# Kernel tuning notes

Measured on AMD Instinct MI355X. Metric: run time of the kernel, lower is better.

## Reference

```python
import jax, jax.numpy as jnp
import numpy as np

N, E, F, H, G, C = 50000, 800000, 768, 256, 512, 2  # H = nhid*2 (nhid=128), G graphs, C classes
NHID = 128


def setup_inputs() -> dict:
    key = jax.random.key(0)
    ks = jax.random.split(key, 18)
    s = 0.05
    x = jax.random.normal(ks[0], (N, F), jnp.float32)
    edge_index = jax.random.randint(ks[1], (2, E), 0, N, dtype=jnp.int32)
    # sorted batch vector; every graph non-empty so the 'first node per graph' gather is valid
    batch = ((jnp.arange(N) * G) // N).astype(jnp.int32)
    return {
        "x": x,
        "edge_index": edge_index,
        "batch": batch,
        # GATConv 1 (in=F, out=H, heads=1)
        "W1": jax.random.normal(ks[2], (F, H), jnp.float32) * s,
        "as1": jax.random.normal(ks[3], (H,), jnp.float32) * s,
        "ad1": jax.random.normal(ks[4], (H,), jnp.float32) * s,
        "b1": jnp.zeros((H,), jnp.float32),
        # GATConv 2 (in=H, out=H)
        "W2": jax.random.normal(ks[5], (H, H), jnp.float32) * s,
        "as2": jax.random.normal(ks[6], (H,), jnp.float32) * s,
        "ad2": jax.random.normal(ks[7], (H,), jnp.float32) * s,
        "b2": jnp.zeros((H,), jnp.float32),
        # fc0: num_features -> nhid (news branch)
        "W0": jax.random.normal(ks[8], (F, NHID), jnp.float32) * s,
        "b0": jnp.zeros((NHID,), jnp.float32),
        # fc1: 2*nhid -> nhid (used twice, as in the source)
        "Wf1": jax.random.normal(ks[9], (H, NHID), jnp.float32) * s,
        "bf1": jnp.zeros((NHID,), jnp.float32),
        # fc2: nhid -> num_classes
        "Wf2": jax.random.normal(ks[10], (NHID, C), jnp.float32) * s,
        "bf2": jnp.zeros((C,), jnp.float32),
    }


def _gat(x, src, dst, W, a_s, a_d, b):
    # PyG GATConv, heads=1, concat=True, negative_slope=0.2, self-loops pre-appended to src/dst.
    h = x @ W                                   # [N, H]
    e = jax.nn.leaky_relu((h @ a_s)[src] + (h @ a_d)[dst], 0.2)  # [E+N]
    m = jax.ops.segment_max(e, dst, num_segments=N)
    ex = jnp.exp(e - m[dst])                    # stable segment softmax numerator
    denom = jax.ops.segment_sum(ex, dst, num_segments=N)
    agg = jax.ops.segment_sum(ex[:, None] * h[src], dst, num_segments=N)  # [N, H]
    return agg / denom[:, None] + b


def reference(x, edge_index, batch, W1, as1, ad1, b1, W2, as2, ad2, b2, W0, b0, Wf1, bf1, Wf2, bf2):
    loop = jnp.arange(N, dtype=edge_index.dtype)
    src = jnp.concatenate([edge_index[0], loop])  # add self-loops (PyG default)
    dst = jnp.concatenate([edge_index[1], loop])
    h = jax.nn.selu(_gat(x, src, dst, W1, as1, ad1, b1))
    h = jax.nn.selu(_gat(h, src, dst, W2, as2, ad2, b2))
    # global mean pool over graphs
    cnt = jax.ops.segment_sum(jnp.ones((N,), h.dtype), batch, num_segments=G)
    pooled = jax.nn.selu(jax.ops.segment_sum(h, batch, num_segments=G) / cnt[:, None])
    z = jax.nn.selu(pooled @ Wf1 + bf1)
    # dropout(p=0.5) in eval mode -> identity
    # concat branch: first node of each graph (news root)
    first_idx = jax.ops.segment_min(jnp.arange(N), batch, num_segments=G)
    news = jax.nn.relu(x[first_idx] @ W0 + b0)
    z = jnp.concatenate([z, news], axis=1)       # [G, 2*nhid]
    z = jax.nn.relu(z @ Wf1 + bf1)
    return jax.nn.log_softmax(z @ Wf2 + bf2, axis=-1)
```

## Files before the change

kernel.cpp:

```cpp
#include <hip/hip_runtime.h>
#include <hip/hip_bf16.h>
#include <cstdint>
#include <cstddef>

#define NN 50000
#define EE 800000
#define FF 768
#define HH 256
#define GG 512
#define CC 2
#define NHIDD 128
#define ETOT (EE + NN)
#define NCHUNK 49

typedef __attribute__((ext_vector_type(8))) short bf16x8;
typedef __attribute__((ext_vector_type(4))) float f32x4;
typedef __attribute__((ext_vector_type(8))) unsigned short us8;

__device__ __forceinline__ float b2f(unsigned short u){
  union { float f; uint32_t i; } v; v.i = ((uint32_t)u) << 16; return v.f;
}
__device__ __forceinline__ unsigned short f2b(float f){
  uint32_t u = __float_as_uint(f);
  uint32_t r = (u + 0x7fffu + ((u >> 16) & 1u)) >> 16;
  return (unsigned short)r;
}
__device__ __forceinline__ float selu_f(float x){
  const float lam = 1.0507009873554805f, alp = 1.6732632423543772f;
  return x > 0.f ? lam * x : lam * alp * (__expf(x) - 1.f);
}

__global__ __launch_bounds__(256) void swizzleW(const float* __restrict__ W,
                                                unsigned short* __restrict__ Wsw, int K){
  int i = blockIdx.x * 256 + threadIdx.x;
  if (i < K * HH){
    int k = i / HH, n = i % HH;
    Wsw[(size_t)(k >> 5) * 8192 + n * 32 + (k & 31)] = f2b(W[i]);
  }
}

__global__ __launch_bounds__(256) void zero_deg(int* deg){
  int i = blockIdx.x * 256 + threadIdx.x;
  if (i < NN) deg[i] = 0;
}

__global__ __launch_bounds__(256) void deg_kernel(const int* __restrict__ dstA, int* __restrict__ deg){
  int i = blockIdx.x * 256 + threadIdx.x;
  if (i < ETOT){
    int d = (i < EE) ? dstA[i] : (i - EE);
    atomicAdd(&deg[d], 1);
  }
}

__global__ __launch_bounds__(256) void scanA(const int* __restrict__ deg, int* __restrict__ bsum){
  __shared__ int red[256];
  int c = blockIdx.x, tid = threadIdx.x;
  int base = c * 1024 + tid * 4;
  int s = 0;
#pragma unroll
  for (int j = 0; j < 4; j++){ int idx = base + j; if (idx < NN) s += deg[idx]; }
  red[tid] = s; __syncthreads();
  for (int off = 128; off > 0; off >>= 1){
    if (tid < off) red[tid] += red[tid + off];
    __syncthreads();
  }
  if (tid == 0) bsum[c] = red[0];
}

__global__ void scanB(int* bsum){
  if (threadIdx.x == 0){
    int run = 0;
    for (int i = 0; i < NCHUNK; i++){ int v = bsum[i]; bsum[i] = run; run += v; }
  }
}

__global__ __launch_bounds__(256) void scanC(const int* __restrict__ deg, const int* __restrict__ bsum,
                                             int* __restrict__ row_ptr, int* __restrict__ fill_ptr){
  __shared__ int ts[256];
  int c = blockIdx.x, tid = threadIdx.x;
  int base = c * 1024 + tid * 4;
  int v[4]; int s = 0;
#pragma unroll
  for (int j = 0; j < 4; j++){ int idx = base + j; v[j] = (idx < NN) ? deg[idx] : 0; s += v[j]; }
  ts[tid] = s; __syncthreads();
  for (int off = 1; off < 256; off <<= 1){
    int add = (tid >= off) ? ts[tid - off] : 0;
    __syncthreads();
    ts[tid] += add;
    __syncthreads();
  }
  int run = ts[tid] - s + bsum[c];
#pragma unroll
  for (int j = 0; j < 4; j++){
    int idx = base + j;
    if (idx < NN){ row_ptr[idx] = run; fill_ptr[idx] = run; }
    run += v[j];
  }
  if (c == 0 && tid == 0) row_ptr[NN] = ETOT;
}

__global__ __launch_bounds__(256) void fill_kernel(const int* __restrict__ srcA, const int* __restrict__ dstA,
                                                   int* __restrict__ fill_ptr, int* __restrict__ csr_src){
  int i = blockIdx.x * 256 + threadIdx.x;
  if (i < ETOT){
    int s = (i < EE) ? srcA[i] : (i - EE);
    int d = (i < EE) ? dstA[i] : (i - EE);
    int pos = atomicAdd(&fill_ptr[d], 1);
    csr_src[pos] = s;
  }
}

template<int K, bool AF32>
__global__ __launch_bounds__(256) void gemm_mfma(const void* __restrict__ Ap,
                                                 const unsigned short* __restrict__ Wsw,
                                                 unsigned short* __restrict__ out, int M){
  __shared__ unsigned short Al[64][40];
  __shared__ unsigned short Bl[256][40];
  const int tid = threadIdx.x;
  const int m0 = blockIdx.x * 64;
  const int lane = tid & 63, w = tid >> 6;
  const int koff = (lane >> 4) * 8;
  const int arow = lane & 15, bcol0 = w * 64 + (lane & 15);
  f32x4 acc[4][4];
#pragma unroll
  for (int rt = 0; rt < 4; rt++)
#pragma unroll
    for (int ct = 0; ct < 4; ct++) acc[rt][ct] = (f32x4){0.f, 0.f, 0.f, 0.f};

  const int srow = tid >> 2, skc = (tid & 3) * 8;
  for (int ks = 0; ks < K / 32; ks++){
    if (m0 + srow < M){
      if (AF32){
        const float* Af = (const float*)Ap;
        size_t ab = (size_t)(m0 + srow) * K + ks * 32 + skc;
        float4 f0 = *(const float4*)&Af[ab];
        float4 f1 = *(const float4*)&Af[ab + 4];
        us8 v;
        v[0] = f2b(f0.x); v[1] = f2b(f0.y); v[2] = f2b(f0.z); v[3] = f2b(f0.w);
        v[4] = f2b(f1.x); v[5] = f2b(f1.y); v[6] = f2b(f1.z); v[7] = f2b(f1.w);
        *(us8*)&Al[srow][skc] = v;
      } else {
        const unsigned short* Au = (const unsigned short*)Ap;
        *(us8*)&Al[srow][skc] = *(const us8*)&Au[(size_t)(m0 + srow) * K + ks * 32 + skc];
      }
    } else {
      us8 z = {0,0,0,0,0,0,0,0}; *(us8*)&Al[srow][skc] = z;
    }
    const unsigned short* wp = Wsw + (size_t)ks * 8192 + tid * 32;
    *(us8*)&Bl[tid][0]  = *(const us8*)&wp[0];
    *(us8*)&Bl[tid][8]  = *(const us8*)&wp[8];
    *(us8*)&Bl[tid][16] = *(const us8*)&wp[16];
    *(us8*)&Bl[tid][24] = *(const us8*)&wp[24];
    __syncthreads();
    bf16x8 af[4], bfr[4];
#pragma unroll
    for (int rt = 0; rt < 4; rt++) af[rt] = *(const bf16x8*)&Al[rt * 16 + arow][koff];
#pragma unroll
    for (int ct = 0; ct < 4; ct++) bfr[ct] = *(const bf16x8*)&Bl[bcol0 + ct * 16][koff];
#pragma unroll
    for (int rt = 0; rt < 4; rt++)
#pragma unroll
      for (int ct = 0; ct < 4; ct++)
        acc[rt][ct] = __builtin_amdgcn_mfma_f32_16x16x32_bf16(af[rt], bfr[ct], acc[rt][ct], 0, 0, 0);
    __syncthreads();
  }
#pragma unroll
  for (int rt = 0; rt < 4; rt++){
    int mbase = m0 + rt * 16 + (lane >> 4) * 4;
#pragma unroll
    for (int r = 0; r < 4; r++){
      int m = mbase + r;
      if (m < M){
        size_t ro = (size_t)m * HH + w * 64 + (lane & 15);
        out[ro + 0]  = f2b(acc[rt][0][r]);
        out[ro + 16] = f2b(acc[rt][1][r]);
        out[ro + 32] = f2b(acc[rt][2][r]);
        out[ro + 48] = f2b(acc[rt][3][r]);
      }
    }
  }
}

__global__ __launch_bounds__(256) void alsald_kernel(const unsigned short* __restrict__ h,
    const float* __restrict__ a_s, const float* __restrict__ a_d,
    float* __restrict__ als, float* __restrict__ ald){
  int node = blockIdx.x * 4 + (threadIdx.x >> 6);
  int lane = threadIdx.x & 63;
  if (node >= NN) return;
  ushort4 hv = *(const ushort4*)&h[(size_t)node * HH + lane * 4];
  float4 as4 = *(const float4*)&a_s[lane * 4];
  float4 ad4 = *(const float4*)&a_d[lane * 4];
  float h0 = b2f(hv.x), h1 = b2f(hv.y), h2 = b2f(hv.z), h3 = b2f(hv.w);
  float s = h0 * as4.x + h1 * as4.y + h2 * as4.z + h3 * as4.w;
  float d = h0 * ad4.x + h1 * ad4.y + h2 * ad4.z + h3 * ad4.w;
  for (int off = 32; off > 0; off >>= 1){ s += __shfl_xor(s, off); d += __shfl_xor(d, off); }
  if (lane == 0){ als[node] = s; ald[node] = d; }
}

__global__ __launch_bounds__(256) void agg_wave(const unsigned short* __restrict__ h,
    const float* __restrict__ als, const float* __restrict__ ald,
    const int* __restrict__ row_ptr, const int* __restrict__ csr_src,
    const float* __restrict__ bias, unsigned short* __restrict__ outp){
  int node = blockIdx.x * 4 + (threadIdx.x >> 6);
  int lane = threadIdx.x & 63;
  if (node >= NN) return;
  int base = row_ptr[node];
  int deg  = row_ptr[node + 1] - base;
  float aldd = ald[node];
  float den = 0.f;
  float a0 = 0.f, a1 = 0.f, a2 = 0.f, a3 = 0.f;
  const size_t fo = (size_t)lane * 4;
  for (int p0 = 0; p0 < deg; p0 += 64){
    int cnt = min(64, deg - p0);
    float ev = 0.f; int s = 0;
    if (lane < cnt){
      s = csr_src[base + p0 + lane];
      float v = als[s] + aldd;
      v = v > 0.f ? v : 0.2f * v;
      ev = __expf(v);
    }
    den += ev;
    int j = 0;
    for (; j + 2 <= cnt; j += 2){
      float e0 = __shfl(ev, j), e1 = __shfl(ev, j + 1);
      int s0 = __shfl(s, j), s1 = __shfl(s, j + 1);
      ushort4 g0 = *(const ushort4*)&h[(size_t)s0 * HH + fo];
      ushort4 g1 = *(const ushort4*)&h[(size_t)s1 * HH + fo];
      a0 += e0 * b2f(g0.x) + e1 * b2f(g1.x);
      a1 += e0 * b2f(g0.y) + e1 * b2f(g1.y);
      a2 += e0 * b2f(g0.z) + e1 * b2f(g1.z);
      a3 += e0 * b2f(g0.w) + e1 * b2f(g1.w);
    }
    for (; j < cnt; j++){
      float e0 = __shfl(ev, j); int s0 = __shfl(s, j);
      ushort4 g0 = *(const ushort4*)&h[(size_t)s0 * HH + fo];
      a0 += e0 * b2f(g0.x); a1 += e0 * b2f(g0.y); a2 += e0 * b2f(g0.z); a3 += e0 * b2f(g0.w);
    }
  }
  for (int off = 32; off > 0; off >>= 1) den += __shfl_xor(den, off);
  float inv = 1.f / den;
  float4 b4 = *(const float4*)&bias[fo];
  ushort4 o;
  o.x = f2b(selu_f(a0 * inv + b4.x));
  o.y = f2b(selu_f(a1 * inv + b4.y));
  o.z = f2b(selu_f(a2 * inv + b4.z));
  o.w = f2b(selu_f(a3 * inv + b4.w));
  *(ushort4*)&outp[(size_t)node * HH + fo] = o;
}

__global__ __launch_bounds__(256) void first_kernel(const int* __restrict__ batch, int* __restrict__ first_idx){
  int n = blockIdx.x * 256 + threadIdx.x;
  if (n < NN){
    int b = batch[n];
    if (n == 0 || batch[n - 1] != b) first_idx[b] = n;
  }
  if (blockIdx.x == 0 && threadIdx.x == 0) first_idx[GG] = NN;
}

__global__ __launch_bounds__(256) void pool_kernel(const unsigned short* __restrict__ x3,
    const int* __restrict__ first_idx, float* __restrict__ pooled){
  int g = blockIdx.x, f = threadIdx.x;
  int s = first_idx[g], e = first_idx[g + 1];
  float acc = 0.f;
  for (int n = s; n < e; n++) acc += b2f(x3[(size_t)n * HH + f]);
  pooled[g * HH + f] = selu_f(acc / (float)(e - s));
}

__global__ __launch_bounds__(128) void z1_kernel(const float* __restrict__ pooled,
    const float* __restrict__ Wf1, const float* __restrict__ bf1,
    float* __restrict__ z1){
  __shared__ float pr[HH];
  int g = blockIdx.x, t = threadIdx.x;
  pr[t] = pooled[g * HH + t];
  pr[t + 128] = pooled[g * HH + t + 128];
  __syncthreads();
  float acc = 0.f;
  for (int k = 0; k < HH; k++) acc += pr[k] * Wf1[k * NHIDD + t];
  z1[g * NHIDD + t] = selu_f(acc + bf1[t]);
}

__global__ __launch_bounds__(128) void news_kernel(const float* __restrict__ x,
    const int* __restrict__ first_idx, const float* __restrict__ W0,
    const float* __restrict__ b0, float* __restrict__ znews){
  __shared__ float xr[FF];
  int g = blockIdx.x, t = threadIdx.x;
  int root = first_idx[g];
  for (int k = t; k < FF; k += 128) xr[k] = x[(size_t)root * FF + k];
  __syncthreads();
  float acc = 0.f;
  for (int k = 0; k < FF; k++) acc += xr[k] * W0[k * NHIDD + t];
  acc += b0[t];
  znews[g * NHIDD + t] = acc > 0.f ? acc : 0.f;
}

__global__ __launch_bounds__(128) void final_kernel(const float* __restrict__ z1,
    const float* __restrict__ znews, const float* __restrict__ Wf1,
    const float* __restrict__ bf1, const float* __restrict__ Wf2,
    const float* __restrict__ bf2, float* __restrict__ out){
  __shared__ float zc[HH];
  __shared__ float l0s[2], l1s[2];
  int g = blockIdx.x, t = threadIdx.x;
  zc[t] = z1[g * NHIDD + t];
  zc[NHIDD + t] = znews[g * NHIDD + t];
  __syncthreads();
  float acc = 0.f;
  for (int k = 0; k < HH; k++) acc += zc[k] * Wf1[k * NHIDD + t];
  float z2 = acc + bf1[t]; z2 = z2 > 0.f ? z2 : 0.f;
  float p0 = z2 * Wf2[t * CC + 0];
  float p1 = z2 * Wf2[t * CC + 1];
  for (int off = 32; off > 0; off >>= 1){ p0 += __shfl_xor(p0, off); p1 += __shfl_xor(p1, off); }
  int lane = t & 63, wid = t >> 6;
  if (lane == 0){ l0s[wid] = p0; l1s[wid] = p1; }
  __syncthreads();
  if (t == 0){
    float l0 = l0s[0] + l0s[1] + bf2[0];
    float l1 = l1s[0] + l1s[1] + bf2[1];
    float mx = fmaxf(l0, l1);
    float lse = mx + logf(__expf(l0 - mx) + __expf(l1 - mx));
    out[g * CC + 0] = l0 - lse;
    out[g * CC + 1] = l1 - lse;
  }
}

extern "C" void kernel_launch(void* const* d_in, const int* in_sizes, int n_in,
                              void* d_out, int out_size, void* d_ws, size_t ws_size,
                              hipStream_t stream){
  const float* x          = (const float*)d_in[0];
  const int* edge_index   = (const int*)d_in[1];
  const int* batch        = (const int*)d_in[2];
  const float* W1  = (const float*)d_in[3];
  const float* as1 = (const float*)d_in[4];
  const float* ad1 = (const float*)d_in[5];
  const float* b1  = (const float*)d_in[6];
  const float* W2  = (const float*)d_in[7];
  const float* as2 = (const float*)d_in[8];
  const float* ad2 = (const float*)d_in[9];
  const float* b2  = (const float*)d_in[10];
  const float* W0  = (const float*)d_in[11];
  const float* b0  = (const float*)d_in[12];
  const float* Wf1 = (const float*)d_in[13];
  const float* bf1 = (const float*)d_in[14];
  const float* Wf2 = (const float*)d_in[15];
  const float* bf2 = (const float*)d_in[16];
  float* out = (float*)d_out;

  char* w = (char*)d_ws;
  size_t off = 0;
  auto alloc = [&](size_t bytes){ size_t o = off; off += (bytes + 255) & ~(size_t)255; return o; };
  unsigned short* h    = (unsigned short*)(w + alloc((size_t)NN * HH * 2));
  unsigned short* x2   = (unsigned short*)(w + alloc((size_t)NN * HH * 2));
  unsigned short* Wsw1 = (unsigned short*)(w + alloc((size_t)FF * HH * 2));
  unsigned short* Wsw2 = (unsigned short*)(w + alloc((size_t)HH * HH * 2));
  float* als     = (float*)(w + alloc((size_t)NN * 4));
  float* ald     = (float*)(w + alloc((size_t)NN * 4));
  int*   deg     = (int*)(w + alloc((size_t)NN * 4));
  int*   row_ptr = (int*)(w + alloc((size_t)(NN + 1) * 4));
  int*   fillp   = (int*)(w + alloc((size_t)NN * 4));
  int*   csr_src = (int*)(w + alloc((size_t)ETOT * 4));
  int*   bsum    = (int*)(w + alloc(64 * 4));
  int*   firsti  = (int*)(w + alloc((size_t)(GG + 1) * 4));
  float* pooled  = (float*)(w + alloc((size_t)GG * HH * 4));
  float* z1      = (float*)(w + alloc((size_t)GG * NHIDD * 4));
  float* znews   = (float*)(w + alloc((size_t)GG * NHIDD * 4));

  const int* srcA = edge_index;
  const int* dstA = edge_index + EE;

  swizzleW<<<(FF * HH + 255) / 256, 256, 0, stream>>>(W1, Wsw1, FF);
  swizzleW<<<(HH * HH + 255) / 256, 256, 0, stream>>>(W2, Wsw2, HH);

  zero_deg<<<(NN + 255) / 256, 256, 0, stream>>>(deg);
  deg_kernel<<<(ETOT + 255) / 256, 256, 0, stream>>>(dstA, deg);
  scanA<<<NCHUNK, 256, 0, stream>>>(deg, bsum);
  scanB<<<1, 64, 0, stream>>>(bsum);
  scanC<<<NCHUNK, 256, 0, stream>>>(deg, bsum, row_ptr, fillp);
  fill_kernel<<<(ETOT + 255) / 256, 256, 0, stream>>>(srcA, dstA, fillp, csr_src);

  const int gemm_grid = (NN + 63) / 64;
  gemm_mfma<FF, true><<<gemm_grid, 256, 0, stream>>>((const void*)x, Wsw1, h, NN);
  alsald_kernel<<<(NN + 3) / 4, 256, 0, stream>>>(h, as1, ad1, als, ald);
  agg_wave<<<(NN + 3) / 4, 256, 0, stream>>>(h, als, ald, row_ptr, csr_src, b1, x2);
  gemm_mfma<HH, false><<<gemm_grid, 256, 0, stream>>>((const void*)x2, Wsw2, h, NN);
  alsald_kernel<<<(NN + 3) / 4, 256, 0, stream>>>(h, as2, ad2, als, ald);
  agg_wave<<<(NN + 3) / 4, 256, 0, stream>>>(h, als, ald, row_ptr, csr_src, b2, x2);
  first_kernel<<<(NN + 255) / 256, 256, 0, stream>>>(batch, firsti);
  pool_kernel<<<GG, 256, 0, stream>>>(x2, firsti, pooled);
  z1_kernel<<<GG, 128, 0, stream>>>(pooled, Wf1, bf1, z1);
  news_kernel<<<GG, 128, 0, stream>>>(x, firsti, W0, b0, znews);
  final_kernel<<<GG, 128, 0, stream>>>(z1, znews, Wf1, bf1, Wf2, bf2, out);
}
```

Measured before the change: 628.1 us.

## Double-buffer A tile and load W fragments directly into registers in GEMM

The MFMA GEMM now double-buffers the A tile in shared memory, prefetching the next k-slice while the current one is computed, so only one barrier per iteration is needed. The weight fragments are no longer staged through shared memory; each lane reads its bf16x8 B fragments straight from global memory into registers and prefetches the next slice. This is meant to hide global load latency and cut LDS traffic and barriers. In exchange, register pressure rises and B is re-read from global/L2 by every block instead of once per block into LDS.

```diff
diff --git a/kernel.cpp b/kernel.cpp
--- a/kernel.cpp
+++ b/kernel.cpp
@@ -114,22 +114,24 @@
 __global__ __launch_bounds__(256) void gemm_mfma(const void* __restrict__ Ap,
                                                  const unsigned short* __restrict__ Wsw,
                                                  unsigned short* __restrict__ out, int M){
-  __shared__ unsigned short Al[64][40];
-  __shared__ unsigned short Bl[256][40];
+  __shared__ unsigned short Al[2][64][40];
   const int tid = threadIdx.x;
   const int m0 = blockIdx.x * 64;
   const int lane = tid & 63, w = tid >> 6;
   const int koff = (lane >> 4) * 8;
-  const int arow = lane & 15, bcol0 = w * 64 + (lane & 15);
+  const int arow = lane & 15;
+  const int nrow = w * 64 + (lane & 15);
+  const int srow = tid >> 2, skc = (tid & 3) * 8;
+  const bool rowok = (m0 + srow < M);
+
   f32x4 acc[4][4];
 #pragma unroll
   for (int rt = 0; rt < 4; rt++)
 #pragma unroll
     for (int ct = 0; ct < 4; ct++) acc[rt][ct] = (f32x4){0.f, 0.f, 0.f, 0.f};
 
-  const int srow = tid >> 2, skc = (tid & 3) * 8;
-  for (int ks = 0; ks < K / 32; ks++){
-    if (m0 + srow < M){
+  auto stageA = [&](int ks, int buf){
+    if (rowok){
       if (AF32){
         const float* Af = (const float*)Ap;
         size_t ab = (size_t)(m0 + srow) * K + ks * 32 + skc;
@@ -138,32 +140,49 @@
         us8 v;
         v[0] = f2b(f0.x); v[1] = f2b(f0.y); v[2] = f2b(f0.z); v[3] = f2b(f0.w);
         v[4] = f2b(f1.x); v[5] = f2b(f1.y); v[6] = f2b(f1.z); v[7] = f2b(f1.w);
-        *(us8*)&Al[srow][skc] = v;
+        *(us8*)&Al[buf][srow][skc] = v;
       } else {
         const unsigned short* Au = (const unsigned short*)Ap;
-        *(us8*)&Al[srow][skc] = *(const us8*)&Au[(size_t)(m0 + srow) * K + ks * 32 + skc];
+        *(us8*)&Al[buf][srow][skc] = *(const us8*)&Au[(size_t)(m0 + srow) * K + ks * 32 + skc];
       }
     } else {
-      us8 z = {0,0,0,0,0,0,0,0}; *(us8*)&Al[srow][skc] = z;
-    }
-    const unsigned short* wp = Wsw + (size_t)ks * 8192 + tid * 32;
-    *(us8*)&Bl[tid][0]  = *(const us8*)&wp[0];
-    *(us8*)&Bl[tid][8]  = *(const us8*)&wp[8];
-    *(us8*)&Bl[tid][16] = *(const us8*)&wp[16];
-    *(us8*)&Bl[tid][24] = *(const us8*)&wp[24];
+      us8 z = {0,0,0,0,0,0,0,0}; *(us8*)&Al[buf][srow][skc] = z;
+    }
+  };
+
+  constexpr int NIT = K / 32;
+  stageA(0, 0);
+  bf16x8 bcur[4];
+  {
+    const unsigned short* bp = Wsw + ((size_t)nrow * 32 + koff);
+#pragma unroll
+    for (int ct = 0; ct < 4; ct++) bcur[ct] = *(const bf16x8*)(bp + ct * 512);
+  }
+  __syncthreads();
+
+  for (int ks = 0; ks < NIT; ks++){
+    bf16x8 bnext[4];
+    if (ks + 1 < NIT){
+      const unsigned short* bp = Wsw + ((size_t)(ks + 1) * 8192 + (size_t)nrow * 32 + koff);
+#pragma unroll
+      for (int ct = 0; ct < 4; ct++) bnext[ct] = *(const bf16x8*)(bp + ct * 512);
+      stageA(ks + 1, (ks + 1) & 1);
+    }
+    bf16x8 af[4];
+#pragma unroll
+    for (int rt = 0; rt < 4; rt++) af[rt] = *(const bf16x8*)&Al[ks & 1][rt * 16 + arow][koff];
+#pragma unroll
+    for (int rt = 0; rt < 4; rt++)
+#pragma unroll
+      for (int ct = 0; ct < 4; ct++)
+        acc[rt][ct] = __builtin_amdgcn_mfma_f32_16x16x32_bf16(af[rt], bcur[ct], acc[rt][ct], 0, 0, 0);
+    if (ks + 1 < NIT){
+#pragma unroll
+      for (int ct = 0; ct < 4; ct++) bcur[ct] = bnext[ct];
+    }
     __syncthreads();
-    bf16x8 af[4], bfr[4];
-#pragma unroll
-    for (int rt = 0; rt < 4; rt++) af[rt] = *(const bf16x8*)&Al[rt * 16 + arow][koff];
-#pragma unroll
-    for (int ct = 0; ct < 4; ct++) bfr[ct] = *(const bf16x8*)&Bl[bcol0 + ct * 16][koff];
-#pragma unroll
-    for (int rt = 0; rt < 4; rt++)
-#pragma unroll
-      for (int ct = 0; ct < 4; ct++)
-        acc[rt][ct] = __builtin_amdgcn_mfma_f32_16x16x32_bf16(af[rt], bfr[ct], acc[rt][ct], 0, 0, 0);
-    __syncthreads();
-  }
+  }
+
 #pragma unroll
   for (int rt = 0; rt < 4; rt++){
     int mbase = m0 + rt * 16 + (lane >> 4) * 4;
```

Result: faster. 613.9 us (-2.3%).
